# Optimization experiments

Measured on AMD Instinct MI355X. Metric: run time of the kernel, lower is better.

Reference implementation:

```python
import jax, jax.numpy as jnp
import numpy as np
from jax import lax

VOCAB = 32000
HID = 1024
SEQ = 4096
EPS = 1e-12  # torch F.normalize default eps


def setup_inputs() -> dict:
    key = jax.random.key(0)
    ks = jax.random.split(key, 6)
    return {
        "src_nums": jax.random.randint(ks[0], (SEQ,), 0, VOCAB),
        "W": 0.01 * jax.random.normal(ks[1], (VOCAB, HID), dtype=jnp.float32),
        "h0": 0.01 * jax.random.normal(ks[2], (HID,), dtype=jnp.float32),
        "W_hi": 0.01 * jax.random.normal(ks[3], (HID, HID), dtype=jnp.float32),
        "W_hh": 0.01 * jax.random.normal(ks[4], (HID, HID), dtype=jnp.float32),
        "b": 0.01 * jax.random.normal(ks[5], (HID,), dtype=jnp.float32),
    }


def reference(src_nums, W, h0, W_hi, W_hh, b):
    # Embedding lookup + L2 normalize over hidden dim (torch F.normalize, dim=1)
    emb = W[src_nums]  # [S, H]
    norm = jnp.maximum(jnp.linalg.norm(emb, axis=1, keepdims=True), EPS)
    emb = emb / norm

    # Sequential tanh RNN recurrence: h_t = tanh(W_hi @ x_t + W_hh @ h_{t-1} + b)
    def step(h, x):
        h_new = jnp.tanh(W_hi @ x + W_hh @ h + b)
        return h_new, h_new

    _, hs = lax.scan(step, h0, emb)  # hs: [S, H]
    return jnp.concatenate([h0[None, :], hs], axis=0)  # [S+1, H]
```

## Files before the change

### kernel.cpp

```cpp
#include <hip/hip_runtime.h>
#include <math.h>

#define HID 1024
#define SEQ 4096
#define NWG 64
#define BT  8

typedef float v4f __attribute__((ext_vector_type(4)));

__global__ void __launch_bounds__(256) embed_gemm(
    const int* __restrict__ src, const float* __restrict__ W,
    const float* __restrict__ Whi, const float* __restrict__ bias,
    float* __restrict__ U) {
  __shared__ float4 se[BT][256];
  __shared__ float  sw[BT][4];

  const int tid  = threadIdx.x;
  const int wv   = tid >> 6;
  const int lane = tid & 63;
  const int t0   = blockIdx.x * BT;

  #pragma unroll
  for (int i = 0; i < BT; i++) {
    const int idx = src[t0 + i];
    float4 v = ((const float4*)(W + (size_t)idx * HID))[tid];
    se[i][tid] = v;
    float ss = v.x*v.x + v.y*v.y + v.z*v.z + v.w*v.w;
    ss += __shfl_xor(ss, 1);  ss += __shfl_xor(ss, 2);  ss += __shfl_xor(ss, 4);
    ss += __shfl_xor(ss, 8);  ss += __shfl_xor(ss, 16); ss += __shfl_xor(ss, 32);
    if (lane == 0) sw[i][wv] = ss;
  }
  __syncthreads();

  float inv_norm[BT];
  #pragma unroll
  for (int i = 0; i < BT; i++) {
    float n = sw[i][0] + sw[i][1] + sw[i][2] + sw[i][3];
    inv_norm[i] = 1.0f / fmaxf(sqrtf(n), 1e-12f);
  }

  float acc[BT][4];
  #pragma unroll
  for (int i = 0; i < BT; i++)
    #pragma unroll
    for (int q = 0; q < 4; q++) acc[i][q] = 0.0f;

  for (int k4 = 0; k4 < HID / 4; k4++) {
    float4 wr[4];
    #pragma unroll
    for (int q = 0; q < 4; q++)
      wr[q] = *(const float4*)(Whi + (size_t)(tid + q * 256) * HID + k4 * 4);
    #pragma unroll
    for (int i = 0; i < BT; i++) {
      float4 e = se[i][k4];
      #pragma unroll
      for (int q = 0; q < 4; q++)
        acc[i][q] += wr[q].x*e.x + wr[q].y*e.y + wr[q].z*e.z + wr[q].w*e.w;
    }
  }

  #pragma unroll
  for (int i = 0; i < BT; i++) {
    #pragma unroll
    for (int q = 0; q < 4; q++) {
      const int j = tid + q * 256;
      U[(size_t)(t0 + i) * HID + j] = acc[i][q] * inv_norm[i] + bias[j];
    }
  }
}

__device__ __forceinline__ bool chk4(const v4f h0v, const v4f h1v,
                                     const v4f h2v, const v4f h3v, float Bc) {
  v4f d0 = h0v - Bc, d1 = h1v - Bc, d2 = h2v - Bc, d3 = h3v - Bc;
  float m0 = fmaxf(fmaxf(fabsf(d0.x), fabsf(d0.y)), fmaxf(fabsf(d0.z), fabsf(d0.w)));
  float m1 = fmaxf(fmaxf(fabsf(d1.x), fabsf(d1.y)), fmaxf(fabsf(d1.z), fabsf(d1.w)));
  float m2 = fmaxf(fmaxf(fabsf(d2.x), fabsf(d2.y)), fmaxf(fabsf(d2.z), fabsf(d2.w)));
  float m3 = fmaxf(fmaxf(fabsf(d3.x), fabsf(d3.y)), fmaxf(fabsf(d3.z), fabsf(d3.w)));
  float m = fmaxf(fmaxf(m0, m1), fmaxf(m2, m3));
  return __all(m < 1.5f) != 0;
}

__device__ __forceinline__ void poll_relay(const float* slotbase, float Bc,
                                           float* dst_lds, int lane,
                                           int* sdead) {
  const float* src = slotbase + 4 * lane;
  v4f A0, A1, A2, A3;
  int tries = 0;
  for (;;) {
    asm volatile(
      "global_load_dwordx4 %0, %4, off sc0 sc1\n\t"
      "global_load_dwordx4 %1, %4, off offset:1024 sc0 sc1\n\t"
      "global_load_dwordx4 %2, %4, off offset:2048 sc0 sc1\n\t"
      "global_load_dwordx4 %3, %4, off offset:3072 sc0 sc1\n\t"
      "s_waitcnt vmcnt(0)"
      : "=&v"(A0), "=&v"(A1), "=&v"(A2), "=&v"(A3)
      : "v"(src) : "memory");
    if (chk4(A0, A1, A2, A3, Bc)) break;
    if (++tries > (1 << 20)) { *sdead = 1; break; }
    __builtin_amdgcn_s_sleep(1);
  }
  A0 -= Bc;  A1 -= Bc;  A2 -= Bc;  A3 -= Bc;
  *(v4f*)(dst_lds +   0 + 4 * lane) = A0;
  *(v4f*)(dst_lds + 256 + 4 * lane) = A1;
  *(v4f*)(dst_lds + 512 + 4 * lane) = A2;
  *(v4f*)(dst_lds + 768 + 4 * lane) = A3;
}

__global__ void __launch_bounds__(256) rnn_seq(
    const float* __restrict__ Whh, const float* __restrict__ U,
    const float* __restrict__ h0, float* __restrict__ out,
    float* __restrict__ hbuf) {
  __shared__ float hsh[2][HID];
  __shared__ int   sdead;

  const int tid   = threadIdx.x;
  const int lane  = tid & 63;
  const int w     = tid >> 6;
  const int b     = blockIdx.x;
  const int r0    = b * 16;
  const int rw    = r0 + w * 4;
  const int myrow = rw + (lane & 3);

  if (tid == 0) sdead = 0;

  if (tid < 16) {
    float rv = h0[r0 + tid];
    out[r0 + tid] = rv;
    float tv = rv + 2.0f;
    const float* dst = hbuf + r0 + tid;
    asm volatile("global_store_dword %0, %1, off sc0 sc1"
                 :: "v"(dst), "v"(tv) : "memory");
  }

  v4f wreg[4][4];
  #pragma unroll
  for (int r = 0; r < 4; r++)
    #pragma unroll
    for (int c = 0; c < 4; c++)
      wreg[r][c] = *(const v4f*)(Whh + (size_t)(rw + r) * HID + c * 256 + 4 * lane);

  float u_cur = U[myrow];

  if (w == 0) poll_relay(hbuf, 2.0f, hsh[0], lane, &sdead);
  __syncthreads();

  #pragma unroll 1
  for (int t = 0; t < SEQ; t++) {
    if (sdead) break;

    const float* hp = hsh[t & 1];
    v4f hd0 = *(const v4f*)(hp +   0 + 4 * lane);
    v4f hd1 = *(const v4f*)(hp + 256 + 4 * lane);
    v4f hd2 = *(const v4f*)(hp + 512 + 4 * lane);
    v4f hd3 = *(const v4f*)(hp + 768 + 4 * lane);

    float a[4];
    #pragma unroll
    for (int r = 0; r < 4; r++) {
      a[r] = wreg[r][0].x*hd0.x + wreg[r][0].y*hd0.y + wreg[r][0].z*hd0.z + wreg[r][0].w*hd0.w
           + wreg[r][1].x*hd1.x + wreg[r][1].y*hd1.y + wreg[r][1].z*hd1.z + wreg[r][1].w*hd1.w
           + wreg[r][2].x*hd2.x + wreg[r][2].y*hd2.y + wreg[r][2].z*hd2.z + wreg[r][2].w*hd2.w
           + wreg[r][3].x*hd3.x + wreg[r][3].y*hd3.y + wreg[r][3].z*hd3.z + wreg[r][3].w*hd3.w;
    }

    #pragma unroll
    for (int m = 1; m <= 32; m <<= 1) {
      a[0] += __shfl_xor(a[0], m);
      a[1] += __shfl_xor(a[1], m);
      a[2] += __shfl_xor(a[2], m);
      a[3] += __shfl_xor(a[3], m);
    }

    float y01 = (lane & 1) ? a[1] : a[0];
    float y23 = (lane & 1) ? a[3] : a[2];
    float y   = (lane & 2) ? y23 : y01;
    const float hn = tanhf(y + u_cur);

    const float Bp = 2.0f + 4.0f * (float)(((t + 1) >> 2) & 1);
    if (lane < 4) {
      out[(size_t)(t + 1) * HID + rw + lane] = hn;
      float tv = hn + Bp;
      const float* dst = hbuf + (((t + 1) & 3) << 10) + rw + lane;
      asm volatile("global_store_dword %0, %1, off sc0 sc1"
                   :: "v"(dst), "v"(tv) : "memory");
    }

    float u_next = U[(size_t)((t + 1 < SEQ) ? t + 1 : t) * HID + myrow];

    if (w == 0 && t + 1 < SEQ)
      poll_relay(hbuf + (((t + 1) & 3) << 10), Bp, hsh[(t + 1) & 1], lane, &sdead);

    __syncthreads();
    u_cur = u_next;
  }
}

extern "C" void kernel_launch(void* const* d_in, const int* in_sizes, int n_in,
                              void* d_out, int out_size, void* d_ws, size_t ws_size,
                              hipStream_t stream) {
  const int*   src = (const int*)  d_in[0];
  const float* W   = (const float*)d_in[1];
  const float* h0  = (const float*)d_in[2];
  const float* Whi = (const float*)d_in[3];
  const float* Whh = (const float*)d_in[4];
  const float* b   = (const float*)d_in[5];
  float* out = (float*)d_out;

  float* U    = (float*)d_ws;
  float* hbuf = (float*)((char*)d_ws + (size_t)SEQ * HID * sizeof(float));

  embed_gemm<<<SEQ / BT, 256, 0, stream>>>(src, W, Whi, b, U);
  rnn_seq<<<NWG, 256, 0, stream>>>(Whh, U, h0, out, hbuf);
}
```

Baseline: 8.600 ms.

## Double-buffer relay polling in asm, use fast tanh, store relay before output

The cross-workgroup hidden-state poll becomes a hand-written asm loop that keeps two sets of loads in flight and checks one while the other arrives, with no sleep between attempts. This aims to cut the latency of the per-step handoff on the serial critical path. It also replaces tanhf with an exp/rcp approximation and issues the relay store before the output store so other workgroups see the new state sooner. The fast tanh changes accuracy slightly, and the hardcoded VGPR clobbers add register pressure and fragility.

```diff
diff --git a/kernel.cpp b/kernel.cpp
--- a/kernel.cpp
+++ b/kernel.cpp
@@ -69,41 +69,154 @@
   }
 }
 
-__device__ __forceinline__ bool chk4(const v4f h0v, const v4f h1v,
-                                     const v4f h2v, const v4f h3v, float Bc) {
-  v4f d0 = h0v - Bc, d1 = h1v - Bc, d2 = h2v - Bc, d3 = h3v - Bc;
-  float m0 = fmaxf(fmaxf(fabsf(d0.x), fabsf(d0.y)), fmaxf(fabsf(d0.z), fabsf(d0.w)));
-  float m1 = fmaxf(fmaxf(fabsf(d1.x), fabsf(d1.y)), fmaxf(fabsf(d1.z), fabsf(d1.w)));
-  float m2 = fmaxf(fmaxf(fabsf(d2.x), fabsf(d2.y)), fmaxf(fabsf(d2.z), fabsf(d2.w)));
-  float m3 = fmaxf(fmaxf(fabsf(d3.x), fabsf(d3.y)), fmaxf(fabsf(d3.z), fabsf(d3.w)));
-  float m = fmaxf(fmaxf(m0, m1), fmaxf(m2, m3));
-  return __all(m < 1.5f) != 0;
-}
-
 __device__ __forceinline__ void poll_relay(const float* slotbase, float Bc,
                                            float* dst_lds, int lane,
                                            int* sdead) {
   const float* src = slotbase + 4 * lane;
-  v4f A0, A1, A2, A3;
-  int tries = 0;
-  for (;;) {
-    asm volatile(
-      "global_load_dwordx4 %0, %4, off sc0 sc1\n\t"
-      "global_load_dwordx4 %1, %4, off offset:1024 sc0 sc1\n\t"
-      "global_load_dwordx4 %2, %4, off offset:2048 sc0 sc1\n\t"
-      "global_load_dwordx4 %3, %4, off offset:3072 sc0 sc1\n\t"
-      "s_waitcnt vmcnt(0)"
-      : "=&v"(A0), "=&v"(A1), "=&v"(A2), "=&v"(A3)
-      : "v"(src) : "memory");
-    if (chk4(A0, A1, A2, A3, Bc)) break;
-    if (++tries > (1 << 20)) { *sdead = 1; break; }
-    __builtin_amdgcn_s_sleep(1);
-  }
-  A0 -= Bc;  A1 -= Bc;  A2 -= Bc;  A3 -= Bc;
-  *(v4f*)(dst_lds +   0 + 4 * lane) = A0;
-  *(v4f*)(dst_lds + 256 + 4 * lane) = A1;
-  *(v4f*)(dst_lds + 512 + 4 * lane) = A2;
-  *(v4f*)(dst_lds + 768 + 4 * lane) = A3;
+  float f0, f1, f2, f3, f4, f5, f6, f7, f8, f9, fa, fb, fc, fd, fe, ff;
+  unsigned df;
+
+#define CHK_SET(BASE0)                                                        \
+      "v_subrev_f32 v28, %[bc], v" #BASE0 "\n\t"
+
+  asm volatile(
+    "global_load_dwordx4 v[32:35], %[src], off sc0 sc1\n\t"
+    "global_load_dwordx4 v[36:39], %[src], off offset:1024 sc0 sc1\n\t"
+    "global_load_dwordx4 v[40:43], %[src], off offset:2048 sc0 sc1\n\t"
+    "global_load_dwordx4 v[44:47], %[src], off offset:3072 sc0 sc1\n\t"
+    "global_load_dwordx4 v[48:51], %[src], off sc0 sc1\n\t"
+    "global_load_dwordx4 v[52:55], %[src], off offset:1024 sc0 sc1\n\t"
+    "global_load_dwordx4 v[56:59], %[src], off offset:2048 sc0 sc1\n\t"
+    "global_load_dwordx4 v[60:63], %[src], off offset:3072 sc0 sc1\n\t"
+    "s_mov_b32 %[df], 0\n\t"
+  "Lpoll%=:\n\t"
+    "s_add_u32 %[df], %[df], 1\n\t"
+    "s_cmp_gt_u32 %[df], 0x40000\n\t"
+    "s_cbranch_scc1 Lbail%=\n\t"
+    "s_waitcnt vmcnt(4)\n\t"
+    "v_subrev_f32 v28, %[bc], v32\n\t"
+    "v_subrev_f32 v29, %[bc], v33\n\t"
+    "v_subrev_f32 v30, %[bc], v34\n\t"
+    "v_max3_f32 v31, |v28|, |v29|, |v30|\n\t"
+    "v_subrev_f32 v28, %[bc], v35\n\t"
+    "v_subrev_f32 v29, %[bc], v36\n\t"
+    "v_subrev_f32 v30, %[bc], v37\n\t"
+    "v_max3_f32 v28, |v28|, |v29|, |v30|\n\t"
+    "v_max_f32 v31, v31, v28\n\t"
+    "v_subrev_f32 v28, %[bc], v38\n\t"
+    "v_subrev_f32 v29, %[bc], v39\n\t"
+    "v_subrev_f32 v30, %[bc], v40\n\t"
+    "v_max3_f32 v28, |v28|, |v29|, |v30|\n\t"
+    "v_max_f32 v31, v31, v28\n\t"
+    "v_subrev_f32 v28, %[bc], v41\n\t"
+    "v_subrev_f32 v29, %[bc], v42\n\t"
+    "v_subrev_f32 v30, %[bc], v43\n\t"
+    "v_max3_f32 v28, |v28|, |v29|, |v30|\n\t"
+    "v_max_f32 v31, v31, v28\n\t"
+    "v_subrev_f32 v28, %[bc], v44\n\t"
+    "v_subrev_f32 v29, %[bc], v45\n\t"
+    "v_subrev_f32 v30, %[bc], v46\n\t"
+    "v_max3_f32 v28, |v28|, |v29|, |v30|\n\t"
+    "v_max_f32 v31, v31, v28\n\t"
+    "v_subrev_f32 v28, %[bc], v47\n\t"
+    "v_max_f32 v31, v31, |v28|\n\t"
+    "v_cmp_le_f32 vcc, 1.5, v31\n\t"
+    "s_cbranch_vccz LdoneA%=\n\t"
+    "global_load_dwordx4 v[32:35], %[src], off sc0 sc1\n\t"
+    "global_load_dwordx4 v[36:39], %[src], off offset:1024 sc0 sc1\n\t"
+    "global_load_dwordx4 v[40:43], %[src], off offset:2048 sc0 sc1\n\t"
+    "global_load_dwordx4 v[44:47], %[src], off offset:3072 sc0 sc1\n\t"
+    "s_waitcnt vmcnt(4)\n\t"
+    "v_subrev_f32 v28, %[bc], v48\n\t"
+    "v_subrev_f32 v29, %[bc], v49\n\t"
+    "v_subrev_f32 v30, %[bc], v50\n\t"
+    "v_max3_f32 v31, |v28|, |v29|, |v30|\n\t"
+    "v_subrev_f32 v28, %[bc], v51\n\t"
+    "v_subrev_f32 v29, %[bc], v52\n\t"
+    "v_subrev_f32 v30, %[bc], v53\n\t"
+    "v_max3_f32 v28, |v28|, |v29|, |v30|\n\t"
+    "v_max_f32 v31, v31, v28\n\t"
+    "v_subrev_f32 v28, %[bc], v54\n\t"
+    "v_subrev_f32 v29, %[bc], v55\n\t"
+    "v_subrev_f32 v30, %[bc], v56\n\t"
+    "v_max3_f32 v28, |v28|, |v29|, |v30|\n\t"
+    "v_max_f32 v31, v31, v28\n\t"
+    "v_subrev_f32 v28, %[bc], v57\n\t"
+    "v_subrev_f32 v29, %[bc], v58\n\t"
+    "v_subrev_f32 v30, %[bc], v59\n\t"
+    "v_max3_f32 v28, |v28|, |v29|, |v30|\n\t"
+    "v_max_f32 v31, v31, v28\n\t"
+    "v_subrev_f32 v28, %[bc], v60\n\t"
+    "v_subrev_f32 v29, %[bc], v61\n\t"
+    "v_subrev_f32 v30, %[bc], v62\n\t"
+    "v_max3_f32 v28, |v28|, |v29|, |v30|\n\t"
+    "v_max_f32 v31, v31, v28\n\t"
+    "v_subrev_f32 v28, %[bc], v63\n\t"
+    "v_max_f32 v31, v31, |v28|\n\t"
+    "v_cmp_le_f32 vcc, 1.5, v31\n\t"
+    "s_cbranch_vccz LdoneB%=\n\t"
+    "global_load_dwordx4 v[48:51], %[src], off sc0 sc1\n\t"
+    "global_load_dwordx4 v[52:55], %[src], off offset:1024 sc0 sc1\n\t"
+    "global_load_dwordx4 v[56:59], %[src], off offset:2048 sc0 sc1\n\t"
+    "global_load_dwordx4 v[60:63], %[src], off offset:3072 sc0 sc1\n\t"
+    "s_branch Lpoll%=\n\t"
+  "LdoneB%=:\n\t"
+    "s_waitcnt vmcnt(0)\n\t"
+    "v_mov_b32 v32, v48\n\t"  "v_mov_b32 v33, v49\n\t"
+    "v_mov_b32 v34, v50\n\t"  "v_mov_b32 v35, v51\n\t"
+    "v_mov_b32 v36, v52\n\t"  "v_mov_b32 v37, v53\n\t"
+    "v_mov_b32 v38, v54\n\t"  "v_mov_b32 v39, v55\n\t"
+    "v_mov_b32 v40, v56\n\t"  "v_mov_b32 v41, v57\n\t"
+    "v_mov_b32 v42, v58\n\t"  "v_mov_b32 v43, v59\n\t"
+    "v_mov_b32 v44, v60\n\t"  "v_mov_b32 v45, v61\n\t"
+    "v_mov_b32 v46, v62\n\t"  "v_mov_b32 v47, v63\n\t"
+    "s_branch Lgood%=\n\t"
+  "LdoneA%=:\n\t"
+    "s_waitcnt vmcnt(0)\n\t"
+  "Lgood%=:\n\t"
+    "s_mov_b32 %[df], 0\n\t"
+    "s_branch Lend%=\n\t"
+  "Lbail%=:\n\t"
+    "s_waitcnt vmcnt(0)\n\t"
+    "s_mov_b32 %[df], 1\n\t"
+  "Lend%=:\n\t"
+    "v_mov_b32 %[f0], v32\n\t"  "v_mov_b32 %[f1], v33\n\t"
+    "v_mov_b32 %[f2], v34\n\t"  "v_mov_b32 %[f3], v35\n\t"
+    "v_mov_b32 %[f4], v36\n\t"  "v_mov_b32 %[f5], v37\n\t"
+    "v_mov_b32 %[f6], v38\n\t"  "v_mov_b32 %[f7], v39\n\t"
+    "v_mov_b32 %[f8], v40\n\t"  "v_mov_b32 %[f9], v41\n\t"
+    "v_mov_b32 %[fa], v42\n\t"  "v_mov_b32 %[fb], v43\n\t"
+    "v_mov_b32 %[fc], v44\n\t"  "v_mov_b32 %[fd], v45\n\t"
+    "v_mov_b32 %[fe], v46\n\t"  "v_mov_b32 %[ff], v47"
+    : [f0]"=v"(f0), [f1]"=v"(f1), [f2]"=v"(f2), [f3]"=v"(f3),
+      [f4]"=v"(f4), [f5]"=v"(f5), [f6]"=v"(f6), [f7]"=v"(f7),
+      [f8]"=v"(f8), [f9]"=v"(f9), [fa]"=v"(fa), [fb]"=v"(fb),
+      [fc]"=v"(fc), [fd]"=v"(fd), [fe]"=v"(fe), [ff]"=v"(ff),
+      [df]"=&s"(df)
+    : [src]"v"(src), [bc]"v"(Bc)
+    : "v28","v29","v30","v31",
+      "v32","v33","v34","v35","v36","v37","v38","v39",
+      "v40","v41","v42","v43","v44","v45","v46","v47",
+      "v48","v49","v50","v51","v52","v53","v54","v55",
+      "v56","v57","v58","v59","v60","v61","v62","v63",
+      "vcc","scc","memory");
+#undef CHK_SET
+
+  if (df) *sdead = 1;
+  v4f o0 = {f0, f1, f2, f3};  o0 -= Bc;
+  v4f o1 = {f4, f5, f6, f7};  o1 -= Bc;
+  v4f o2 = {f8, f9, fa, fb};  o2 -= Bc;
+  v4f o3 = {fc, fd, fe, ff};  o3 -= Bc;
+  *(v4f*)(dst_lds +   0 + 4 * lane) = o0;
+  *(v4f*)(dst_lds + 256 + 4 * lane) = o1;
+  *(v4f*)(dst_lds + 512 + 4 * lane) = o2;
+  *(v4f*)(dst_lds + 768 + 4 * lane) = o3;
+}
+
+__device__ __forceinline__ float tanh_fast(float x) {
+  x = fminf(fmaxf(x, -15.0f), 15.0f);
+  float e = __expf(2.0f * x);
+  return 1.0f - 2.0f * __builtin_amdgcn_rcpf(e + 1.0f);
 }
 
 __global__ void __launch_bounds__(256) rnn_seq(
@@ -174,15 +287,15 @@
     float y01 = (lane & 1) ? a[1] : a[0];
     float y23 = (lane & 1) ? a[3] : a[2];
     float y   = (lane & 2) ? y23 : y01;
-    const float hn = tanhf(y + u_cur);
+    const float hn = tanh_fast(y + u_cur);
 
     const float Bp = 2.0f + 4.0f * (float)(((t + 1) >> 2) & 1);
     if (lane < 4) {
-      out[(size_t)(t + 1) * HID + rw + lane] = hn;
       float tv = hn + Bp;
       const float* dst = hbuf + (((t + 1) & 3) << 10) + rw + lane;
       asm volatile("global_store_dword %0, %1, off sc0 sc1"
                    :: "v"(dst), "v"(tv) : "memory");
+      out[(size_t)(t + 1) * HID + rw + lane] = hn;
     }
 
     float u_next = U[(size_t)((t + 1 < SEQ) ? t + 1 : t) * HID + myrow];
```

New measurement: 11.06 ms. +28.6%, slower.
